# Performance work log

Measured on AMD Instinct MI355X. Metric: run time of the kernel, lower is better.

Reference implementation:

```python
import jax, jax.numpy as jnp
import numpy as np

NUM_HEADS = 12


def get_rel_pos(q_size, k_size, rel_pos):
    # relative coordinate lookup (q_size == k_size here; table has 2*size >= 2*size-1 rows)
    idx = jnp.arange(q_size)[:, None] - jnp.arange(k_size)[None, :] + (k_size - 1)
    return rel_pos[idx]  # [q_size, k_size, head_dim]


def setup_inputs() -> dict:
    key = jax.random.key(0)
    ks = jax.random.split(key, 5)
    B, H, W, E = 8, 32, 32, 768
    hd = E // NUM_HEADS
    x = jax.random.normal(ks[0], (B, H, W, E), jnp.float32)
    Wqkv = jax.random.normal(ks[1], (E, 3 * E), jnp.float32) * (E ** -0.5)
    bqkv = jnp.zeros((3 * E,), jnp.float32)
    Wproj = jax.random.normal(ks[2], (E, E), jnp.float32) * (E ** -0.5)
    bproj = jnp.zeros((E,), jnp.float32)
    rel_pos_h = jax.random.normal(ks[3], (2 * H, hd), jnp.float32) * 0.02
    rel_pos_w = jax.random.normal(ks[4], (2 * W, hd), jnp.float32) * 0.02
    return dict(x=x, Wqkv=Wqkv, bqkv=bqkv, Wproj=Wproj, bproj=bproj,
                rel_pos_h=rel_pos_h, rel_pos_w=rel_pos_w)


def reference(x, Wqkv, bqkv, Wproj, bproj, rel_pos_h, rel_pos_w):
    B, H, W, E = x.shape
    nh = NUM_HEADS
    hd = E // nh
    N = H * W
    scale = hd ** -0.5
    # QKV projection, then the exact reshape/transpose sequence of the TF module
    qkv = x.reshape(B, N, E) @ Wqkv + bqkv                       # [B, N, 3E]
    qkv = qkv.reshape(B, N, nh, hd, 3).transpose(0, 1, 2, 4, 3)  # [B, N, nh, 3, hd]
    qkv = qkv.reshape(B * nh, N, hd, 3)                          # raw row-major reshape (faithful)
    q, k, v = qkv[..., 0], qkv[..., 1], qkv[..., 2]              # each [B*nh, N, hd]
    attn = jnp.einsum('bnd,bmd->bnm', q * scale, k)              # [B*nh, N, N]
    # decomposed relative position bias (SAM-style)
    Rh = get_rel_pos(H, H, rel_pos_h)                            # [H, H, hd]
    Rw = get_rel_pos(W, W, rel_pos_w)                            # [W, W, hd]
    r_q = q.reshape(B * nh, H, W, hd)
    rel_h = jnp.einsum('bhwc,hkc->bhwk', r_q, Rh)                # [B*nh, H, W, H]
    rel_w = jnp.einsum('bhwc,wkc->bhwk', r_q, Rw)                # [B*nh, H, W, W]
    attn = (attn.reshape(B * nh, H, W, H, W)
            + rel_h[..., :, None]
            + rel_w[..., None, :]).reshape(B * nh, N, N)
    attn = jax.nn.softmax(attn, axis=-1)
    out = attn @ v                                               # [B*nh, N, hd]
    # faithful raw reshape + transpose back to [B, H, W, E]
    out = out.reshape(B, H, W, nh, hd).transpose(0, 3, 1, 2, 4).reshape(B, H, W, nh * hd)
    return out @ Wproj + bproj
```

## Files before the change

kernel.cpp:

```cpp
#include <hip/hip_runtime.h>
#include <hip/hip_bf16.h>


typedef __attribute__((ext_vector_type(8))) short short8;
typedef __attribute__((ext_vector_type(4))) float f32x4;

__global__ __launch_bounds__(256) void cast_f32_bf16(const float* __restrict__ in,
                                                     __hip_bfloat16* __restrict__ out) {
  int i = (blockIdx.x * 256 + threadIdx.x) * 4;
  float4 v = *(const float4*)&in[i];
  out[i + 0] = __float2bfloat16(v.x);
  out[i + 1] = __float2bfloat16(v.y);
  out[i + 2] = __float2bfloat16(v.z);
  out[i + 3] = __float2bfloat16(v.w);
}

__global__ __launch_bounds__(256) void transpose_cast(const float* __restrict__ in,
                                                      __hip_bfloat16* __restrict__ out,
                                                      int K, int N) {
  __shared__ float tile[32][33];
  int n0 = blockIdx.x * 32, k0 = blockIdx.y * 32;
  int tx = threadIdx.x & 31, ty = threadIdx.x >> 5;
#pragma unroll
  for (int i = 0; i < 4; ++i)
    tile[ty + i * 8][tx] = in[(size_t)(k0 + ty + i * 8) * N + n0 + tx];
  __syncthreads();
#pragma unroll
  for (int i = 0; i < 4; ++i)
    out[(size_t)(n0 + ty + i * 8) * K + k0 + tx] = __float2bfloat16(tile[tx][ty + i * 8]);
}

__device__ inline void gload16(const void* g, void* l) {
  __builtin_amdgcn_global_load_lds((const __attribute__((address_space(1))) void*)g,
                                   (__attribute__((address_space(3))) void*)l, 16, 0, 0);
}

template<int BM, bool OUT_BF16>
__global__ __launch_bounds__(256) void gemm_dma(const __hip_bfloat16* __restrict__ A,
                                                const __hip_bfloat16* __restrict__ Bt,
                                                const float* __restrict__ bias,
                                                void* __restrict__ Cout,
                                                int N, int K) {
  constexpr int FM = BM / 32;
  __shared__ __hip_bfloat16 Al[BM * 64];
  __shared__ __hip_bfloat16 Bl[128 * 64];
  int n0 = blockIdx.x * 128, m0 = blockIdx.y * BM;
  int tid = threadIdx.x, lane = tid & 63, wid = tid >> 6;
  int wm = wid >> 1, wn = wid & 1;
  int lr = lane & 15, lg = lane >> 4;
  int row_l = lane >> 3, col8 = (lane & 7) * 8;
  f32x4 acc[FM][4] = {};
  for (int k0 = 0; k0 < K; k0 += 64) {
#pragma unroll
    for (int j = 0; j < BM / 32; ++j) {
      int jj = wid * (BM / 32) + j;
      int arow = jj * 8 + row_l;
      gload16(&A[(size_t)(m0 + arow) * K + k0 + col8], &Al[jj * 512]);
    }
#pragma unroll
    for (int j = 0; j < 4; ++j) {
      int jj = wid * 4 + j;
      int brow = jj * 8 + row_l;
      gload16(&Bt[(size_t)(n0 + brow) * K + k0 + col8], &Bl[jj * 512]);
    }
    __syncthreads();
#pragma unroll
    for (int ks = 0; ks < 2; ++ks) {
      short8 af[FM], bfr[4];
#pragma unroll
      for (int m = 0; m < FM; ++m)
        af[m] = *(const short8*)&Al[(wm * (BM / 2) + m * 16 + lr) * 64 + ks * 32 + lg * 8];
#pragma unroll
      for (int n = 0; n < 4; ++n)
        bfr[n] = *(const short8*)&Bl[(wn * 64 + n * 16 + lr) * 64 + ks * 32 + lg * 8];
#pragma unroll
      for (int m = 0; m < FM; ++m)
#pragma unroll
        for (int n = 0; n < 4; ++n)
          acc[m][n] = __builtin_amdgcn_mfma_f32_16x16x32_bf16(af[m], bfr[n], acc[m][n], 0, 0, 0);
    }
    __syncthreads();
  }
#pragma unroll
  for (int n = 0; n < 4; ++n) {
    int col = n0 + wn * 64 + n * 16 + lr;
    float bv = bias[col];
#pragma unroll
    for (int m = 0; m < FM; ++m) {
      int rowb = m0 + wm * (BM / 2) + m * 16 + lg * 4;
#pragma unroll
      for (int r = 0; r < 4; ++r) {
        float v = acc[m][n][r] + bv;
        if (OUT_BF16)
          ((__hip_bfloat16*)Cout)[(size_t)(rowb + r) * N + col] = __float2bfloat16(v);
        else
          ((float*)Cout)[(size_t)(rowb + r) * N + col] = v;
      }
    }
  }
}

__global__ __launch_bounds__(256) void permute_v2(const __hip_bfloat16* __restrict__ qkv,
                                                  __hip_bfloat16* __restrict__ Q,
                                                  __hip_bfloat16* __restrict__ Kd,
                                                  __hip_bfloat16* __restrict__ Vt) {
  int bh = blockIdx.y, n0 = blockIdx.x * 64;
  int tid = threadIdx.x;
  __shared__ short raw[64 * 200];
  __shared__ short vt[64][72];
  const short* src = (const short*)qkv + (size_t)(bh * 1024 + n0) * 192;
#pragma unroll
  for (int i = 0; i < 6; ++i) {
    int c16 = tid + i * 256;
    int wi = c16 / 24, off = (c16 % 24) * 8;
    *(short8*)&raw[wi * 200 + off] = *(const short8*)&src[(size_t)c16 * 8];
  }
  __syncthreads();
  int wi = tid >> 2, g4 = tid & 3;
  const short* rw_ = &raw[wi * 200];
  short8 qv[2], kv_[2];
#pragma unroll
  for (int half = 0; half < 2; ++half)
#pragma unroll
    for (int j = 0; j < 8; ++j) {
      int d2 = g4 * 16 + half * 8 + j;
      int u = 3 * d2;
      qv[half][j]  = rw_[((u) & 63) * 3 + ((u) >> 6)];
      kv_[half][j] = rw_[((u + 1) & 63) * 3 + ((u + 1) >> 6)];
      vt[d2][wi]   = rw_[((u + 2) & 63) * 3 + ((u + 2) >> 6)];
    }
  size_t base = (size_t)bh * 65536 + (size_t)(n0 + wi) * 64 + g4 * 16;
  *(short8*)&Q[base] = qv[0];
  *(short8*)&Q[base + 8] = qv[1];
  *(short8*)&Kd[base] = kv_[0];
  *(short8*)&Kd[base + 8] = kv_[1];
  __syncthreads();
  int d2r = tid >> 2;
  size_t vbase = (size_t)bh * 65536 + (size_t)d2r * 1024 + n0 + g4 * 16;
  *(short8*)&Vt[vbase]     = *(const short8*)&vt[d2r][g4 * 16];
  *(short8*)&Vt[vbase + 8] = *(const short8*)&vt[d2r][g4 * 16 + 8];
}

__device__ inline short8 cvt8(const float* p) {
  short8 r;
#pragma unroll
  for (int j = 0; j < 8; ++j) {
    __hip_bfloat16 b = __float2bfloat16(p[j]);
    r[j] = *reinterpret_cast<const short*>(&b);
  }
  return r;
}

__device__ inline unsigned packtrunc(float a, float b) {
  return __builtin_amdgcn_perm(__float_as_uint(b), __float_as_uint(a), 0x07060302u);
}

#define L2E 1.44269504088896f
__global__ __launch_bounds__(512) void attn13(const __hip_bfloat16* __restrict__ Q,
                                              const __hip_bfloat16* __restrict__ Kd,
                                              const __hip_bfloat16* __restrict__ Vt,
                                              const float* __restrict__ rph,
                                              const float* __restrict__ rpw,
                                              __hip_bfloat16* __restrict__ outp) {
  int orig = blockIdx.x;
  int xcd = orig & 7, loc = orig >> 3;
  int bh = xcd * 12 + (loc % 12);
  int qt = loc / 12;
  int tid = threadIdx.x;
  int lane = tid & 63, w = tid >> 6;
  int lr = lane & 15, lg = lane >> 4;
  int xr = lr & 7;

  __shared__ __align__(16) char lds[49152];

  const __hip_bfloat16* Qb = Q + (size_t)bh * 65536;
  const __hip_bfloat16* Kb = Kd + (size_t)bh * 65536;
  const __hip_bfloat16* Vb = Vt + (size_t)bh * 65536;

  int q0 = qt * 128 + w * 16;
  int hq = q0 >> 5;
  int wq_lane = (q0 & 31) + lr;

  short8 qf0 = *(const short8*)&Qb[(size_t)(q0 + lr) * 64 + lg * 8];
  short8 qf1 = *(const short8*)&Qb[(size_t)(q0 + lr) * 64 + 32 + lg * 8];

  char* rhb = lds + 24576 + w * 1024;
#pragma unroll
  for (int kt = 0; kt < 2; ++kt) {
    int row = hq - (kt * 16 + lr) + 31;
    const float* tp = rph + (size_t)row * 64 + lg * 8;
    short8 th0 = cvt8(tp), th1 = cvt8(tp + 32);
    f32x4 a = {};
    a = __builtin_amdgcn_mfma_f32_16x16x32_bf16(qf0, th0, a, 0, 0, 0);
    a = __builtin_amdgcn_mfma_f32_16x16x32_bf16(qf1, th1, a, 0, 0, 0);
#pragma unroll
    for (int r = 0; r < 4; ++r) {
      int q = lg * 4 + r;
      int e = kt * 16 + lr;
      int sw = ((e >> 1) ^ q) << 2;
      *(__hip_bfloat16*)(rhb + q * 64 + sw + (e & 1) * 2) = __float2bfloat16(a[r] * L2E);
    }
  }
  __hip_bfloat16* rwt = (__hip_bfloat16*)(lds + w * 2176);
#pragma unroll
  for (int jt = 0; jt < 4; ++jt) {
    const float* tp = rpw + (size_t)(jt * 16 + lr) * 64 + lg * 8;
    short8 tw0 = cvt8(tp), tw1 = cvt8(tp + 32);
    f32x4 a = {};
    a = __builtin_amdgcn_mfma_f32_16x16x32_bf16(qf0, tw0, a, 0, 0, 0);
    a = __builtin_amdgcn_mfma_f32_16x16x32_bf16(qf1, tw1, a, 0, 0, 0);
#pragma unroll
    for (int r = 0; r < 4; ++r)
      rwt[(lg * 4 + r) * 68 + jt * 16 + lr] = __float2bfloat16(a[r] * L2E);
  }
  float rwreg[8];
#pragma unroll
  for (int i = 0; i < 8; ++i) {
    int k = (i >> 2) * 16 + lg * 4 + (i & 3);
    rwreg[i] = __bfloat162float(rwt[lr * 68 + (wq_lane - k + 31)]);
  }
  __syncthreads();

  f32x4 O[4] = {};
  float m_ = -1e30f, lsum = 0.f;
  const float C = 0.125f * L2E;
  char* pc = lds + 32768 + w * 2048;
  char* vcb = lds + 16384;

  int g_ = lane >> 3;
  int colb = ((lane & 7) ^ g_) * 8;

  gload16(&Kb[(size_t)(w * 8 + g_) * 64 + colb], lds + w * 1024);

  int cur = 0;
#pragma unroll 1
  for (int kv0 = 0; kv0 < 1024; kv0 += 64) {
    __builtin_amdgcn_sched_barrier(0);
    __builtin_amdgcn_s_barrier();
    gload16(&Vb[(size_t)(w * 8 + g_) * 1024 + kv0 + colb], vcb + w * 1024);
    int nkv = (kv0 + 64 < 1024) ? kv0 + 64 : 960;
    gload16(&Kb[(size_t)(nkv + w * 8 + g_) * 64 + colb], lds + (cur ^ 1) * 8192 + w * 1024);
    asm volatile("s_waitcnt vmcnt(2)" ::: "memory");
    __builtin_amdgcn_sched_barrier(0);
    __builtin_amdgcn_s_barrier();
    __builtin_amdgcn_sched_barrier(0);

    const char* kc = lds + cur * 8192;
    short8 kf[8];
#pragma unroll
    for (int t = 0; t < 4; ++t)
#pragma unroll
      for (int h = 0; h < 2; ++h)
        kf[2 * t + h] = *(const short8*)(kc + (t * 16 + lr) * 128 + (((h * 4 + lg) ^ xr) * 16));
    f32x4 st[4];
#pragma unroll
    for (int t = 0; t < 4; ++t) {
      f32x4 z = {};
      z = __builtin_amdgcn_mfma_f32_16x16x32_bf16(kf[2 * t], qf0, z, 0, 0, 0);
      z = __builtin_amdgcn_mfma_f32_16x16x32_bf16(kf[2 * t + 1], qf1, z, 0, 0, 0);
      st[t] = z;
    }
    int s_ = kv0 >> 6;
    unsigned bu = *(const unsigned*)(rhb + lr * 64 + ((s_ ^ lr) << 2));
    float bh0 = __uint_as_float(bu << 16);
    float bh1 = __uint_as_float(bu & 0xffff0000u);
    float mx = -1e30f;
#pragma unroll
    for (int t = 0; t < 4; ++t)
#pragma unroll
      for (int r = 0; r < 4; ++r) {
        float sv = fmaf(st[t][r], C, ((t < 2) ? bh0 : bh1) + rwreg[(t & 1) * 4 + r]);
        st[t][r] = sv;
        mx = fmaxf(mx, sv);
      }
    if (!__all(mx <= m_ + 8.f)) {
      float mw = fmaxf(mx, __shfl_xor(mx, 16, 64));
      mw = fmaxf(mw, __shfl_xor(mw, 32, 64));
      float mnew = fmaxf(m_, mw);
      float al = exp2f(m_ - mnew);
      lsum *= al;
      m_ = mnew;
#pragma unroll
      for (int r = 0; r < 4; ++r) {
        float av = __shfl(al, lg * 4 + r, 64);
#pragma unroll
        for (int dt = 0; dt < 4; ++dt) O[dt][r] *= av;
      }
    }
    float sa = 0.f;
#pragma unroll
    for (int t = 0; t < 4; ++t) {
      float p0 = exp2f(st[t][0] - m_);
      float p1 = exp2f(st[t][1] - m_);
      float p2 = exp2f(st[t][2] - m_);
      float p3 = exp2f(st[t][3] - m_);
      sa += (p0 + p1) + (p2 + p3);
      uint2 wv;
      wv.x = packtrunc(p0, p1);
      wv.y = packtrunc(p2, p3);
      int slot = (2 * t + (lg >> 1)) ^ xr;
      *(uint2*)(pc + lr * 128 + slot * 16 + (lg & 1) * 8) = wv;
    }
    lsum += sa;
    short8 pf0 = *(const short8*)(pc + lr * 128 + (((0 + lg) ^ xr) * 16));
    short8 pf1 = *(const short8*)(pc + lr * 128 + (((4 + lg) ^ xr) * 16));
    asm volatile("s_waitcnt vmcnt(1)" ::: "memory");
    __builtin_amdgcn_sched_barrier(0);
    __builtin_amdgcn_s_barrier();
    __builtin_amdgcn_sched_barrier(0);
#pragma unroll
    for (int dt = 0; dt < 4; ++dt) {
      short8 vf0 = *(const short8*)(vcb + (dt * 16 + lr) * 128 + (((0 + lg) ^ xr) * 16));
      short8 vf1 = *(const short8*)(vcb + (dt * 16 + lr) * 128 + (((4 + lg) ^ xr) * 16));
      O[dt] = __builtin_amdgcn_mfma_f32_16x16x32_bf16(pf0, vf0, O[dt], 0, 0, 0);
      O[dt] = __builtin_amdgcn_mfma_f32_16x16x32_bf16(pf1, vf1, O[dt], 0, 0, 0);
    }
    cur ^= 1;
  }

  float lt = lsum;
  lt += __shfl_xor(lt, 16, 64);
  lt += __shfl_xor(lt, 32, 64);
  float linv = 1.f / lt;
#pragma unroll
  for (int r = 0; r < 4; ++r) {
    float lv = __shfl(linv, lg * 4 + r, 64);
    int n = q0 + lg * 4 + r;
#pragma unroll
    for (int dt = 0; dt < 4; ++dt) {
      int d = dt * 16 + lr;
      int Sidx = bh * 65536 + n * 64 + d;
      int b = Sidx / 786432, r1 = Sidx % 786432;
      int pp = r1 / 24576, r2 = r1 % 24576;
      int qq = r2 / 768, r3 = r2 % 768;
      int j = r3 >> 6, dd = r3 & 63;
      int P = b * 786432 + j * 65536 + pp * 2048 + qq * 64 + dd;
      outp[P] = __float2bfloat16(O[dt][r] * lv);
    }
  }
}

extern "C" void kernel_launch(void* const* d_in, const int* in_sizes, int n_in,
                              void* d_out, int out_size, void* d_ws, size_t ws_size,
                              hipStream_t stream) {
  const float* x     = (const float*)d_in[0];
  const float* Wqkv  = (const float*)d_in[1];
  const float* bqkv  = (const float*)d_in[2];
  const float* Wproj = (const float*)d_in[3];
  const float* bproj = (const float*)d_in[4];
  const float* rph   = (const float*)d_in[5];
  const float* rpw   = (const float*)d_in[6];
  float* out = (float*)d_out;
  char* ws = (char*)d_ws;

  __hip_bfloat16* xb     = (__hip_bfloat16*)(ws);
  __hip_bfloat16* wqkvT  = (__hip_bfloat16*)(ws + 12582912);
  __hip_bfloat16* wprojT = (__hip_bfloat16*)(ws + 16121856);
  __hip_bfloat16* qkvb   = (__hip_bfloat16*)(ws + 17301504);
  __hip_bfloat16* Qm     = (__hip_bfloat16*)(ws + 55050240);
  __hip_bfloat16* Km     = (__hip_bfloat16*)(ws + 67633152);
  __hip_bfloat16* Vtm    = (__hip_bfloat16*)(ws + 80216064);

  cast_f32_bf16<<<dim3(6144), dim3(256), 0, stream>>>(x, xb);
  transpose_cast<<<dim3(72, 24), dim3(256), 0, stream>>>(Wqkv, wqkvT, 768, 2304);
  transpose_cast<<<dim3(24, 24), dim3(256), 0, stream>>>(Wproj, wprojT, 768, 768);
  gemm_dma<128, true><<<dim3(18, 64), dim3(256), 0, stream>>>(xb, wqkvT, bqkv, (void*)qkvb, 2304, 768);
  permute_v2<<<dim3(16, 96), dim3(256), 0, stream>>>(qkvb, Qm, Km, Vtm);
  attn13<<<dim3(768), dim3(512), 0, stream>>>(Qm, Km, Vtm, rph, rpw, qkvb);
  gemm_dma<64, false><<<dim3(6, 128), dim3(256), 0, stream>>>(qkvb, wprojT, bproj, (void*)out, 768, 768);
}
```

Measured before the change: 174.7 us.

## Double-buffer GEMM LDS tiles with async prefetch and XOR-swizzled layout

```diff
diff --git a/kernel.cpp b/kernel.cpp
--- a/kernel.cpp
+++ b/kernel.cpp
@@ -36,50 +36,83 @@
 }
 
 template<int BM, bool OUT_BF16>
-__global__ __launch_bounds__(256) void gemm_dma(const __hip_bfloat16* __restrict__ A,
-                                                const __hip_bfloat16* __restrict__ Bt,
-                                                const float* __restrict__ bias,
-                                                void* __restrict__ Cout,
-                                                int N, int K) {
+__global__ __launch_bounds__(256) void gemm_pipe(const __hip_bfloat16* __restrict__ A,
+                                                 const __hip_bfloat16* __restrict__ Bt,
+                                                 const float* __restrict__ bias,
+                                                 void* __restrict__ Cout,
+                                                 int N, int K) {
   constexpr int FM = BM / 32;
-  __shared__ __hip_bfloat16 Al[BM * 64];
-  __shared__ __hip_bfloat16 Bl[128 * 64];
+  constexpr int ABYTES = BM * 128;
+  constexpr int AOPW = BM / 32;
+  __shared__ __align__(16) char lds[2 * ABYTES + 2 * 16384];
+  char* Abuf = lds;
+  char* Bbuf = lds + 2 * ABYTES;
   int n0 = blockIdx.x * 128, m0 = blockIdx.y * BM;
   int tid = threadIdx.x, lane = tid & 63, wid = tid >> 6;
   int wm = wid >> 1, wn = wid & 1;
   int lr = lane & 15, lg = lane >> 4;
-  int row_l = lane >> 3, col8 = (lane & 7) * 8;
+  int xr = lr & 7;
+  int g_ = lane >> 3;
+  int colsw = ((lane & 7) ^ g_) * 8;
   f32x4 acc[FM][4] = {};
+
+#pragma unroll
+  for (int j = 0; j < AOPW; ++j) {
+    int op = wid * AOPW + j;
+    gload16(&A[(size_t)(m0 + op * 8 + g_) * K + colsw], Abuf + op * 1024);
+  }
+#pragma unroll
+  for (int j = 0; j < 4; ++j) {
+    int op = wid * 4 + j;
+    gload16(&Bt[(size_t)(n0 + op * 8 + g_) * K + colsw], Bbuf + op * 1024);
+  }
+
+  int cur = 0;
+#pragma unroll 1
   for (int k0 = 0; k0 < K; k0 += 64) {
-#pragma unroll
-    for (int j = 0; j < BM / 32; ++j) {
-      int jj = wid * (BM / 32) + j;
-      int arow = jj * 8 + row_l;
-      gload16(&A[(size_t)(m0 + arow) * K + k0 + col8], &Al[jj * 512]);
+    __builtin_amdgcn_sched_barrier(0);
+    __builtin_amdgcn_s_barrier();
+    int kn = (k0 + 64 < K) ? k0 + 64 : k0;
+#pragma unroll
+    for (int j = 0; j < AOPW; ++j) {
+      int op = wid * AOPW + j;
+      gload16(&A[(size_t)(m0 + op * 8 + g_) * K + kn + colsw],
+              Abuf + (cur ^ 1) * ABYTES + op * 1024);
     }
 #pragma unroll
     for (int j = 0; j < 4; ++j) {
-      int jj = wid * 4 + j;
-      int brow = jj * 8 + row_l;
-      gload16(&Bt[(size_t)(n0 + brow) * K + k0 + col8], &Bl[jj * 512]);
-    }
-    __syncthreads();
+      int op = wid * 4 + j;
+      gload16(&Bt[(size_t)(n0 + op * 8 + g_) * K + kn + colsw],
+              Bbuf + (cur ^ 1) * 16384 + op * 1024);
+    }
+    if constexpr (BM == 128) asm volatile("s_waitcnt vmcnt(8)" ::: "memory");
+    else                     asm volatile("s_waitcnt vmcnt(6)" ::: "memory");
+    __builtin_amdgcn_sched_barrier(0);
+    __builtin_amdgcn_s_barrier();
+    __builtin_amdgcn_sched_barrier(0);
+
+    const char* Ac = Abuf + cur * ABYTES;
+    const char* Bc = Bbuf + cur * 16384;
 #pragma unroll
     for (int ks = 0; ks < 2; ++ks) {
       short8 af[FM], bfr[4];
 #pragma unroll
-      for (int m = 0; m < FM; ++m)
-        af[m] = *(const short8*)&Al[(wm * (BM / 2) + m * 16 + lr) * 64 + ks * 32 + lg * 8];
-#pragma unroll
-      for (int n = 0; n < 4; ++n)
-        bfr[n] = *(const short8*)&Bl[(wn * 64 + n * 16 + lr) * 64 + ks * 32 + lg * 8];
+      for (int m = 0; m < FM; ++m) {
+        int row = wm * (BM / 2) + m * 16 + lr;
+        af[m] = *(const short8*)(Ac + row * 128 + (((ks * 4 + lg) ^ xr) * 16));
+      }
+#pragma unroll
+      for (int n = 0; n < 4; ++n) {
+        int row = wn * 64 + n * 16 + lr;
+        bfr[n] = *(const short8*)(Bc + row * 128 + (((ks * 4 + lg) ^ xr) * 16));
+      }
 #pragma unroll
       for (int m = 0; m < FM; ++m)
 #pragma unroll
         for (int n = 0; n < 4; ++n)
           acc[m][n] = __builtin_amdgcn_mfma_f32_16x16x32_bf16(af[m], bfr[n], acc[m][n], 0, 0, 0);
     }
-    __syncthreads();
+    cur ^= 1;
   }
 #pragma unroll
   for (int n = 0; n < 4; ++n) {
@@ -364,8 +397,8 @@
   cast_f32_bf16<<<dim3(6144), dim3(256), 0, stream>>>(x, xb);
   transpose_cast<<<dim3(72, 24), dim3(256), 0, stream>>>(Wqkv, wqkvT, 768, 2304);
   transpose_cast<<<dim3(24, 24), dim3(256), 0, stream>>>(Wproj, wprojT, 768, 768);
-  gemm_dma<128, true><<<dim3(18, 64), dim3(256), 0, stream>>>(xb, wqkvT, bqkv, (void*)qkvb, 2304, 768);
+  gemm_pipe<128, true><<<dim3(18, 64), dim3(256), 0, stream>>>(xb, wqkvT, bqkv, (void*)qkvb, 2304, 768);
   permute_v2<<<dim3(16, 96), dim3(256), 0, stream>>>(qkvb, Qm, Km, Vtm);
   attn13<<<dim3(768), dim3(512), 0, stream>>>(Qm, Km, Vtm, rph, rpw, qkvb);
-  gemm_dma<64, false><<<dim3(6, 128), dim3(256), 0, stream>>>(qkvb, wprojT, bproj, (void*)out, 768, 768);
-}
+  gemm_pipe<64, false><<<dim3(6, 128), dim3(256), 0, stream>>>(qkvb, wprojT, bproj, (void*)out, 768, 768);
+}
```

After: 153.2 us. 1.14x faster.
